# Performance work log

Hardware: AMD Instinct MI355X
Metric: run time of the kernel (lower is better)

The kernel has to match this reference:

```python
import jax, jax.numpy as jnp
import numpy as np
from functools import partial

B, N, T = 4, 10000, 128
E = 160000
H, C = 4, 64            # heads, out_channels per head
GAT_DIM = H * C         # 256
NEG_SLOPE = 0.2


def conv1d(x, w, b):
    # x: (M, Cin, L), w: (Cout, Cin, K), 'same' padding (pad=1 for k=3)
    y = jax.lax.conv_general_dilated(x, w, window_strides=(1,), padding=[(1, 1)],
                                     dimension_numbers=('NCH', 'OIH', 'NCH'))
    return y + b[None, :, None]


def maxpool2(x):
    # kernel=2, stride=2 over last axis
    return jax.lax.reduce_window(x, -jnp.inf, jax.lax.max,
                                 (1, 1, 2), (1, 1, 2), 'VALID')


def gat_layer_single(x, src, dst, W, att_s, att_d, bias):
    # x: (N, Fin); PyG GATConv with concat=True, self-loops already appended to src/dst
    n = x.shape[0]
    xl = (x @ W).reshape(n, H, C)                       # (N, H, C)
    a_s = jnp.sum(xl * att_s[None], axis=-1)            # (N, H)
    a_d = jnp.sum(xl * att_d[None], axis=-1)            # (N, H)
    e = jax.nn.leaky_relu(a_s[src] + a_d[dst], NEG_SLOPE)  # (E', H)
    emax = jax.ops.segment_max(e, dst, num_segments=n)     # (N, H)
    ex = jnp.exp(e - emax[dst])
    denom = jax.ops.segment_sum(ex, dst, num_segments=n)   # (N, H)
    alpha = ex / (denom[dst] + 1e-16)                       # (E', H)
    msg = xl[src] * alpha[..., None]                        # (E', H, C)
    out = jax.ops.segment_sum(msg, dst, num_segments=n)     # (N, H, C)
    return out.reshape(n, H * C) + bias


def setup_inputs() -> dict:
    key = jax.random.key(0)
    ks = jax.random.split(key, 24)
    rn = lambda k, sh, fan: jax.random.normal(k, sh, jnp.float32) / np.sqrt(fan)
    inp = {
        'x': jax.random.normal(ks[0], (B, N, T), jnp.float32),
        'edge_index': jax.random.randint(ks[1], (2, E), 0, N, jnp.int64),
        # temporal conv
        'cw1': rn(ks[2], (32, 1, 3), 3), 'cb1': jnp.zeros((32,), jnp.float32),
        'cw2': rn(ks[3], (64, 32, 3), 96), 'cb2': jnp.zeros((64,), jnp.float32),
        # GAT layer 0 (in=64)
        'W0': rn(ks[4], (64, GAT_DIM), 64), 'as0': rn(ks[5], (H, C), C), 'ad0': rn(ks[6], (H, C), C),
        'b0': jnp.zeros((GAT_DIM,), jnp.float32),
        # GAT layer 1 (in=256)
        'W1': rn(ks[7], (GAT_DIM, GAT_DIM), GAT_DIM), 'as1': rn(ks[8], (H, C), C), 'ad1': rn(ks[9], (H, C), C),
        'b1': jnp.zeros((GAT_DIM,), jnp.float32),
        # classification head 256->128->2
        'Wc1': rn(ks[10], (GAT_DIM, 128), GAT_DIM), 'bc1': jnp.zeros((128,), jnp.float32),
        'Wc2': rn(ks[11], (128, 2), 128), 'bc2': jnp.zeros((2,), jnp.float32),
        # attribution head 256->64->1
        'Wa1': rn(ks[12], (GAT_DIM, 64), GAT_DIM), 'ba1': jnp.zeros((64,), jnp.float32),
        'Wa2': rn(ks[13], (64, 1), 64), 'ba2': jnp.zeros((1,), jnp.float32),
    }
    return inp


def reference(x, edge_index, cw1, cb1, cw2, cb2, W0, as0, ad0, b0, W1, as1, ad1, b1,
              Wc1, bc1, Wc2, bc2, Wa1, ba1, Wa2, ba2):
    b, n, t = x.shape
    # ---- temporal conv over all B*N node signals ----
    xf = x.reshape(b * n, 1, t)
    h = jax.nn.relu(conv1d(xf, cw1, cb1))            # (BN, 32, T)
    h = maxpool2(h)                                  # (BN, 32, T//2)
    h = jax.nn.relu(conv1d(h, cw2, cb2))             # (BN, 64, T//2)
    feat = jnp.mean(h, axis=-1).reshape(b, n, 64)    # adaptive_avg_pool1d(1)
    # ---- GAT stack (self-loops appended, PyG default) ----
    src0, dst0 = edge_index[0], edge_index[1]
    loops = jnp.arange(n, dtype=src0.dtype)
    src = jnp.concatenate([src0, loops])
    dst = jnp.concatenate([dst0, loops])
    gat0 = jax.vmap(partial(gat_layer_single, src=src, dst=dst, W=W0, att_s=as0, att_d=ad0, bias=b0))
    gat1 = jax.vmap(partial(gat_layer_single, src=src, dst=dst, W=W1, att_s=as1, att_d=ad1, bias=b1))
    g = jax.nn.relu(gat0(feat))                      # (B, N, 256); dropout = identity (eval)
    g = jax.nn.relu(gat1(g))                         # (B, N, 256)
    # ---- heads ----
    pooled = jnp.mean(g, axis=1)                     # (B, 256)
    logits = jax.nn.relu(pooled @ Wc1 + bc1) @ Wc2 + bc2          # (B, 2)
    attr = jax.nn.sigmoid(jax.nn.relu(g @ Wa1 + ba1) @ Wa2 + ba2)  # (B, N, 1)
    return logits, attr[..., 0]
```

## Files before the change

### kernel.cpp

```cpp
#include <hip/hip_runtime.h>
#include <hip/hip_bf16.h>
#include <math.h>

typedef __hip_bfloat16 bf16;
typedef unsigned short u16;
typedef unsigned int u32;
typedef __attribute__((ext_vector_type(8))) short short8;
typedef __attribute__((ext_vector_type(4))) float f32x4;
typedef __attribute__((ext_vector_type(2))) float f32x2;

#define BATCH 4
#define NNODE 10000
#define TLEN 128
#define NEDGE 160000
#define GDIM 256
#define NHEAD 4

#define S_CW1 0
#define S_CB1 96
#define S_CB2 128
#define S_AS0 192
#define S_AD0 448
#define S_B0  704
#define S_AS1 960
#define S_AD1 1216
#define S_B1  1472
#define S_BC1 1728
#define S_WC2 1856
#define S_BC2 2112
#define S_BA1 2114
#define S_WA2 2178
#define S_BA2 2242
#define S_TOTAL 2243

__device__ __forceinline__ float prelu(float v) { return fmaxf(v, 0.f); }
__device__ __forceinline__ u16 f2b(float f) {
    union { float f; u32 u; } v; v.f = f;
    u32 r = v.u + 0x7FFF + ((v.u >> 16) & 1);
    return (u16)(r >> 16);
}
__device__ __forceinline__ float u2f(u16 u) {
    union { u32 u; float f; } v; v.u = ((u32)u) << 16;
    return v.f;
}
__device__ __forceinline__ float ldw(const void* p, int off, bool isbf) {
    return isbf ? u2f(((const u16*)p)[off]) : ((const float*)p)[off];
}

__device__ __forceinline__ bool probe_x_bf16(const void* xsrc) {
    int lane = threadIdx.x & 63;
    u16 h = ((const u16*)xsrc)[2 * lane];
    int e = (h >> 7) & 0xFF;
    unsigned long long m = __ballot(e >= 117 && e <= 130);
    return __popcll(m) >= 32;
}
__device__ __forceinline__ bool probe_ei64(const int* ei) {
    int lane = threadIdx.x & 63;
    int v = ei[2 * lane + 1];
    unsigned long long m = __ballot(v == 0);
    return __popcll(m) >= 56;
}

struct WPtrs { const void* p[20]; };

#define PRE_TBLK 665
__global__ __launch_bounds__(256) void k_pre(WPtrs wp, const void* __restrict__ xsrc,
        const int* __restrict__ ei, float* __restrict__ wbuf,
        u16* __restrict__ cw2r, u16* __restrict__ W0t, u16* __restrict__ W1t,
        u16* __restrict__ Wa1t, int* __restrict__ counts) {
    bool isbf = probe_x_bf16(xsrc);
    int b = blockIdx.x;
    if (b >= PRE_TBLK) {
        const int C2[16] = {0,96,128,192,448,704,960,1216,1472,1728,1856,2112,
                            2114,2178,2242,2243};
        const int SRC[15] = {0,1,3,5,6,7,9,10,11,13,14,15,17,18,19};
        int i = (b - PRE_TBLK) * 256 + threadIdx.x;
        if (i >= S_TOTAL) return;
        int j = 14;
        for (int t = 0; t < 15; ++t) { if (i < C2[t + 1]) { j = t; break; } }
        wbuf[i] = ldw(wp.p[SRC[j]], i - C2[j], isbf);
        return;
    }
    int i = b * 256 + threadIdx.x;
    if (i < 6144) {
        int c2 = i / 96, k = i - c2 * 96, s = k >> 5, ci = k & 31;
        cw2r[i] = f2b(ldw(wp.p[2], c2 * 96 + ci * 3 + s, isbf));
    }
    if (i < 16384) {
        int k = i >> 8, c = i & 255;
        W0t[c * 64 + k] = f2b(ldw(wp.p[4], k * 256 + c, isbf));
        int ka = i >> 6, ca = i & 63;
        Wa1t[ca * 256 + ka] = f2b(ldw(wp.p[16], ka * 64 + ca, isbf));
    }
    if (i < 65536) {
        int k = i >> 8, c = i & 255;
        W1t[c * 256 + k] = f2b(ldw(wp.p[8], k * 256 + c, isbf));
    }
    if (i < NEDGE + NNODE) {
        bool ei64 = probe_ei64(ei);
        int dst;
        if (i < NEDGE) dst = ei64 ? ei[2 * (NEDGE + i)] : ei[NEDGE + i];
        else dst = i - NEDGE;
        if (dst >= 0 && dst < NNODE) atomicAdd(&counts[dst], 1);
    }
}

__global__ __launch_bounds__(1024) void k_scan(const int* __restrict__ counts,
        int* __restrict__ cur, int* __restrict__ row_ptr) {
    __shared__ int buf[1024];
    int t = threadIdx.x;
    int base = t * 10;
    int c[10];
    int s = 0;
    #pragma unroll
    for (int i = 0; i < 10; ++i) {
        int idx = base + i;
        c[i] = (idx < NNODE) ? counts[idx] : 0;
        s += c[i];
    }
    buf[t] = s;
    __syncthreads();
    for (int off = 1; off < 1024; off <<= 1) {
        int v = (t >= off) ? buf[t - off] : 0;
        __syncthreads();
        buf[t] += v;
        __syncthreads();
    }
    int run = buf[t] - s;
    #pragma unroll
    for (int i = 0; i < 10; ++i) {
        int idx = base + i;
        if (idx < NNODE) {
            cur[idx] = run;
            run += c[i];
            row_ptr[idx + 1] = run;
        }
    }
    if (t == 0) row_ptr[0] = 0;
}

#define HSTR 40
#define FSTR 72
#define NPW 4
#define FILL_BLK 665
__global__ __launch_bounds__(256) void k_conv(const void* __restrict__ xsrc,
        const float* __restrict__ wbuf, const u16* __restrict__ cw2r,
        const u16* __restrict__ W0t, u16* __restrict__ featb,
        u16* __restrict__ xlb, float* __restrict__ a_s, float* __restrict__ a_d,
        const int* __restrict__ ei, int* __restrict__ cur, int* __restrict__ col_src) {
    __shared__ __align__(16) float xs[4][132];
    __shared__ float w1s[96], b1s[32], b2s[64];
    __shared__ __align__(16) u16 hb[4][66 * HSTR];
    __shared__ __align__(16) u16 fs[16][FSTR];

    bool isbf = probe_x_bf16(xsrc);
    int tid = threadIdx.x;
    int wave = tid >> 6, lane = tid & 63;
    int node0 = blockIdx.x * (4 * NPW);

    int m = lane & 15, q = lane >> 4;
    short8 bfr[4][3];
    #pragma unroll
    for (int nt = 0; nt < 4; ++nt)
        #pragma unroll
        for (int sh = 0; sh < 3; ++sh)
            bfr[nt][sh] = *(const short8*)&cw2r[(nt * 16 + m) * 96 + sh * 32 + q * 8];

    if (tid < 96) w1s[tid] = wbuf[S_CW1 + tid];
    if (tid < 32) b1s[tid] = wbuf[S_CB1 + tid];
    if (tid < 64) b2s[tid] = wbuf[S_CB2 + tid];
    if (tid < 8) xs[tid >> 1][(tid & 1) ? 129 : 0] = 0.f;
    if (tid < 64) {
        int w = tid >> 4, idx = tid & 15;
        *(u32*)&hb[w][2 * idx] = 0;
        *(u32*)&hb[w][65 * HSTR + 2 * idx] = 0;
    }
    __syncthreads();

    float* xsw = xs[wave];
    u16* hw = &hb[wave][0];

    int d = m, uu = q;
    float wa0 = w1s[6 * d + 0], wa1 = w1s[6 * d + 1], wa2 = w1s[6 * d + 2];
    float wb0 = w1s[6 * d + 3], wb1 = w1s[6 * d + 4], wb2 = w1s[6 * d + 5];
    float ba = b1s[2 * d], bb = b1s[2 * d + 1];
    float b2vv[4];
    #pragma unroll
    for (int nt = 0; nt < 4; ++nt) b2vv[nt] = b2s[nt * 16 + m];

    int node = node0 + wave;
    u32 plo = 0; float2 pf = {0.f, 0.f};
    if (isbf) plo = ((const u32*)xsrc)[(size_t)node * 64 + lane];
    else      pf  = ((const float2*)xsrc)[(size_t)node * 64 + lane];

    for (int j = 0; j < NPW; ++j) {
        if (isbf) {
            xsw[1 + 2 * lane] = u2f((u16)(plo & 0xFFFF));
            xsw[2 + 2 * lane] = u2f((u16)(plo >> 16));
        } else {
            xsw[1 + 2 * lane] = pf.x;
            xsw[2 + 2 * lane] = pf.y;
        }
        if (j + 1 < NPW) {
            int nxt = node + 4;
            if (isbf) plo = ((const u32*)xsrc)[(size_t)nxt * 64 + lane];
            else      pf  = ((const float2*)xsrc)[(size_t)nxt * 64 + lane];
        }

        #pragma unroll
        for (int it = 0; it < 16; ++it) {
            int u = uu + 4 * it;
            int t0 = 2 * u;
            float2 xa = *(const float2*)&xsw[t0];
            float2 xb = *(const float2*)&xsw[t0 + 2];
            float x0 = xa.x, x1 = xa.y, x2 = xb.x, x3 = xb.y;
            f32x2 A = {x0, x1}, Bv = {x1, x2}, Cv = {x2, x3};
            f32x2 va = {ba, ba}; va += wa0 * A; va += wa1 * Bv; va += wa2 * Cv;
            f32x2 vb = {bb, bb}; vb += wb0 * A; vb += wb1 * Bv; vb += wb2 * Cv;
            float ha = fmaxf(fmaxf(va.x, va.y), 0.f);
            float hb2 = fmaxf(fmaxf(vb.x, vb.y), 0.f);
            __hip_bfloat162 hp2 = __float22bfloat162_rn(make_float2(ha, hb2));
            u32 pack; __builtin_memcpy(&pack, &hp2, 4);
            *(u32*)&hw[(u + 1) * HSTR + 2 * d] = pack;
        }

        float pc0 = 0.f, pc1 = 0.f, pc2 = 0.f, pc3 = 0.f;
        #pragma unroll
        for (int mt = 0; mt < 4; ++mt) {
            const u16* hr = &hw[(mt * 16 + m) * HSTR + q * 8];
            short8 a0 = *(const short8*)&hr[0 * HSTR];
            short8 a1 = *(const short8*)&hr[1 * HSTR];
            short8 a2 = *(const short8*)&hr[2 * HSTR];
            f32x4 c0 = {0.f,0.f,0.f,0.f}, c1 = {0.f,0.f,0.f,0.f};
            f32x4 c2 = {0.f,0.f,0.f,0.f}, c3 = {0.f,0.f,0.f,0.f};
            c0 = __builtin_amdgcn_mfma_f32_16x16x32_bf16(a0, bfr[0][0], c0, 0, 0, 0);
            c1 = __builtin_amdgcn_mfma_f32_16x16x32_bf16(a0, bfr[1][0], c1, 0, 0, 0);
            c2 = __builtin_amdgcn_mfma_f32_16x16x32_bf16(a0, bfr[2][0], c2, 0, 0, 0);
            c3 = __builtin_amdgcn_mfma_f32_16x16x32_bf16(a0, bfr[3][0], c3, 0, 0, 0);
            c0 = __builtin_amdgcn_mfma_f32_16x16x32_bf16(a1, bfr[0][1], c0, 0, 0, 0);
            c1 = __builtin_amdgcn_mfma_f32_16x16x32_bf16(a1, bfr[1][1], c1, 0, 0, 0);
            c2 = __builtin_amdgcn_mfma_f32_16x16x32_bf16(a1, bfr[2][1], c2, 0, 0, 0);
            c3 = __builtin_amdgcn_mfma_f32_16x16x32_bf16(a1, bfr[3][1], c3, 0, 0, 0);
            c0 = __builtin_amdgcn_mfma_f32_16x16x32_bf16(a2, bfr[0][2], c0, 0, 0, 0);
            c1 = __builtin_amdgcn_mfma_f32_16x16x32_bf16(a2, bfr[1][2], c1, 0, 0, 0);
            c2 = __builtin_amdgcn_mfma_f32_16x16x32_bf16(a2, bfr[2][2], c2, 0, 0, 0);
            c3 = __builtin_amdgcn_mfma_f32_16x16x32_bf16(a2, bfr[3][2], c3, 0, 0, 0);
            pc0 += prelu(c0[0] + b2vv[0]) + prelu(c0[1] + b2vv[0])
                 + prelu(c0[2] + b2vv[0]) + prelu(c0[3] + b2vv[0]);
            pc1 += prelu(c1[0] + b2vv[1]) + prelu(c1[1] + b2vv[1])
                 + prelu(c1[2] + b2vv[1]) + prelu(c1[3] + b2vv[1]);
            pc2 += prelu(c2[0] + b2vv[2]) + prelu(c2[1] + b2vv[2])
                 + prelu(c2[2] + b2vv[2]) + prelu(c2[3] + b2vv[2]);
            pc3 += prelu(c3[0] + b2vv[3]) + prelu(c3[1] + b2vv[3])
                 + prelu(c3[2] + b2vv[3]) + prelu(c3[3] + b2vv[3]);
        }
        pc0 += __shfl_xor(pc0, 16, 64); pc0 += __shfl_xor(pc0, 32, 64);
        pc1 += __shfl_xor(pc1, 16, 64); pc1 += __shfl_xor(pc1, 32, 64);
        pc2 += __shfl_xor(pc2, 16, 64); pc2 += __shfl_xor(pc2, 32, 64);
        pc3 += __shfl_xor(pc3, 16, 64); pc3 += __shfl_xor(pc3, 32, 64);
        float v = (q == 0) ? pc0 : (q == 1) ? pc1 : (q == 2) ? pc2 : pc3;
        u16 fv = f2b(v * (1.f / 64.f));
        if (node < 32) featb[(size_t)node * 64 + lane] = fv;
        fs[wave + 4 * j][lane] = fv;

        node += 4;
    }

    if (blockIdx.x < FILL_BLK) {
        bool ei64 = probe_ei64(ei);
        int e = blockIdx.x * 256 + tid;
        if (e < NEDGE + NNODE) {
            int src, dst;
            if (e < NEDGE) {
                if (ei64) { src = ei[2 * e]; dst = ei[2 * (NEDGE + e)]; }
                else      { src = ei[e];     dst = ei[NEDGE + e]; }
            } else {
                src = dst = e - NEDGE;
            }
            if (dst >= 0 && dst < NNODE) {
                int pos = atomicAdd(&cur[dst], 1);
                if (pos >= 0 && pos < NEDGE + NNODE) col_src[pos] = src;
            }
        }
    }

    __syncthreads();

    {
        f32x4 acc[4];
        #pragma unroll
        for (int ntl = 0; ntl < 4; ++ntl) acc[ntl] = {0.f, 0.f, 0.f, 0.f};
        #pragma unroll
        for (int kc = 0; kc < 64; kc += 32) {
            short8 a = *(const short8*)&fs[m][kc + q * 8];
            #pragma unroll
            for (int ntl = 0; ntl < 4; ++ntl) {
                int col0 = wave * 64 + ntl * 16;
                short8 bw = *(const short8*)&W0t[(size_t)(col0 + m) * 64 + kc + q * 8];
                acc[ntl] = __builtin_amdgcn_mfma_f32_16x16x32_bf16(a, bw, acc[ntl], 0, 0, 0);
            }
        }
        #pragma unroll
        for (int ntl = 0; ntl < 4; ++ntl) {
            #pragma unroll
            for (int r = 0; r < 4; ++r)
                xlb[(size_t)(node0 + q * 4 + r) * 256 + wave * 64 + ntl * 16 + m]
                    = f2b(acc[ntl][r]);
        }
        const float* asw_p = wbuf + S_AS0;
        const float* adw_p = wbuf + S_AD0;
        float sh_s[4] = {0, 0, 0, 0}, sh_d[4] = {0, 0, 0, 0};
        #pragma unroll
        for (int ntl = 0; ntl < 4; ++ntl) {
            float asw = asw_p[wave * 64 + ntl * 16 + m];
            float adw = adw_p[wave * 64 + ntl * 16 + m];
            #pragma unroll
            for (int r = 0; r < 4; ++r) {
                sh_s[r] += acc[ntl][r] * asw;
                sh_d[r] += acc[ntl][r] * adw;
            }
        }
        #pragma unroll
        for (int off = 1; off < 16; off <<= 1) {
            #pragma unroll
            for (int r = 0; r < 4; ++r) {
                sh_s[r] += __shfl_xor(sh_s[r], off, 64);
                sh_d[r] += __shfl_xor(sh_d[r], off, 64);
            }
        }
        if (m == 0) {
            int bb2 = node0 / NNODE;
            int nn0 = node0 - bb2 * NNODE;
            #pragma unroll
            for (int r = 0; r < 4; ++r) {
                int nn = nn0 + q * 4 + r;
                a_s[(size_t)nn * 16 + bb2 * 4 + wave] = sh_s[r];
                a_d[(size_t)nn * 16 + bb2 * 4 + wave] = sh_d[r];
            }
        }
    }
}

#define GSTR 264
__global__ __launch_bounds__(512) void k_agg_gemm(const u16* __restrict__ xlb,
        const float* __restrict__ a_s, const float* __restrict__ a_d,
        const int* __restrict__ row_ptr, const int* __restrict__ col_src,
        const float* __restrict__ bias, const u16* __restrict__ W1t,
        const float* __restrict__ wbuf, u16* __restrict__ outb,
        float* __restrict__ as_out, float* __restrict__ ad_out) {
    __shared__ __align__(16) u16 gt[16][GSTR];
    __shared__ float ps_s[8][16], ps_d[8][16];

    int tid = threadIdx.x;
    int wave = tid >> 6, lane = tid & 63;
    int dl = wave >> 1;
    int dst = __builtin_amdgcn_readfirstlane(blockIdx.x * 4 + dl);
    int bp = (wave & 1) * 2;
    int beg = __builtin_amdgcn_readfirstlane(row_ptr[dst]);
    int end = __builtin_amdgcn_readfirstlane(row_ptr[dst + 1]);

    int bl = lane >> 5;
    int s = lane & 31;
    int h = s >> 3;
    int b = bp + bl;
    int asoff = b * 4 + h;
    size_t rowb = (size_t)b * NNODE;
    float advh = a_d[(size_t)dst * 16 + asoff];

    float m = -INFINITY, l = 0.f;
    float acc[8];
    #pragma unroll
    for (int k = 0; k < 8; ++k) acc[k] = 0.f;

    int i = beg;
    int n0 = 0, n1 = 0, n2 = 0, n3 = 0;
    if (i + 4 <= end) {
        n0 = col_src[i]; n1 = col_src[i + 1];
        n2 = col_src[i + 2]; n3 = col_src[i + 3];
    }
    while (i + 4 <= end) {
        int s0 = min(max(n0, 0), NNODE - 1);
        int s1 = min(max(n1, 0), NNODE - 1);
        int s2 = min(max(n2, 0), NNODE - 1);
        int s3 = min(max(n3, 0), NNODE - 1);
        float a0 = a_s[(size_t)s0 * 16 + asoff];
        float a1 = a_s[(size_t)s1 * 16 + asoff];
        float a2 = a_s[(size_t)s2 * 16 + asoff];
        float a3 = a_s[(size_t)s3 * 16 + asoff];
        short8 x0 = *(const short8*)&xlb[(rowb + s0) * 256 + s * 8];
        short8 x1 = *(const short8*)&xlb[(rowb + s1) * 256 + s * 8];
        short8 x2 = *(const short8*)&xlb[(rowb + s2) * 256 + s * 8];
        short8 x3 = *(const short8*)&xlb[(rowb + s3) * 256 + s * 8];
        i += 4;
        if (i + 4 <= end) {
            n0 = col_src[i]; n1 = col_src[i + 1];
            n2 = col_src[i + 2]; n3 = col_src[i + 3];
        }
        float e0 = a0 + advh; e0 = (e0 >= 0.f) ? e0 : 0.2f * e0;
        float e1 = a1 + advh; e1 = (e1 >= 0.f) ? e1 : 0.2f * e1;
        float e2 = a2 + advh; e2 = (e2 >= 0.f) ? e2 : 0.2f * e2;
        float e3 = a3 + advh; e3 = (e3 >= 0.f) ? e3 : 0.2f * e3;
        float cmax = fmaxf(fmaxf(e0, e1), fmaxf(e2, e3));
        if (__any(cmax > m)) {
            float mn = fmaxf(m, cmax);
            float r = __expf(m - mn);
            m = mn;
            l *= r;
            #pragma unroll
            for (int k = 0; k < 8; ++k) acc[k] *= r;
        }
        float p0 = __expf(e0 - m); l += p0;
        #pragma unroll
        for (int k = 0; k < 8; ++k) acc[k] += p0 * u2f((u16)x0[k]);
        float p1 = __expf(e1 - m); l += p1;
        #pragma unroll
        for (int k = 0; k < 8; ++k) acc[k] += p1 * u2f((u16)x1[k]);
        float p2 = __expf(e2 - m); l += p2;
        #pragma unroll
        for (int k = 0; k < 8; ++k) acc[k] += p2 * u2f((u16)x2[k]);
        float p3 = __expf(e3 - m); l += p3;
        #pragma unroll
        for (int k = 0; k < 8; ++k) acc[k] += p3 * u2f((u16)x3[k]);
    }
    for (; i < end; ++i) {
        int s0 = min(max(col_src[i], 0), NNODE - 1);
        float a0 = a_s[(size_t)s0 * 16 + asoff];
        short8 x0 = *(const short8*)&xlb[(rowb + s0) * 256 + s * 8];
        float e0 = a0 + advh; e0 = (e0 >= 0.f) ? e0 : 0.2f * e0;
        if (__any(e0 > m)) {
            float mn = fmaxf(m, e0);
            float r = __expf(m - mn);
            m = mn;
            l *= r;
            #pragma unroll
            for (int k = 0; k < 8; ++k) acc[k] *= r;
        }
        float p0 = __expf(e0 - m); l += p0;
        #pragma unroll
        for (int k = 0; k < 8; ++k) acc[k] += p0 * u2f((u16)x0[k]);
    }

    float rl = 1.f / (l + 1e-16f);
    short8 o;
    #pragma unroll
    for (int k = 0; k < 8; ++k)
        o[k] = (short)f2b(prelu(acc[k] * rl + bias[s * 8 + k]));
    int grow = dl * 4 + b;
    *(short8*)&gt[grow][s * 8] = o;
    __syncthreads();

    int mm = lane & 15, q = lane >> 4;
    f32x4 ac2[2];
    ac2[0] = {0.f, 0.f, 0.f, 0.f};
    ac2[1] = {0.f, 0.f, 0.f, 0.f};
    for (int kc = 0; kc < 256; kc += 32) {
        short8 a = *(const short8*)&gt[mm][kc + q * 8];
        #pragma unroll
        for (int ntl = 0; ntl < 2; ++ntl) {
            short8 bw = *(const short8*)&W1t[(size_t)(wave * 32 + ntl * 16 + mm) * 256 + kc + q * 8];
            ac2[ntl] = __builtin_amdgcn_mfma_f32_16x16x32_bf16(a, bw, ac2[ntl], 0, 0, 0);
        }
    }
    int dbase = blockIdx.x * 4;
    #pragma unroll
    for (int ntl = 0; ntl < 2; ++ntl) {
        #pragma unroll
        for (int r = 0; r < 4; ++r)
            outb[((size_t)r * NNODE + dbase + q) * 256 + wave * 32 + ntl * 16 + mm]
                = f2b(ac2[ntl][r]);
    }
    float sh_s[4] = {0, 0, 0, 0}, sh_d[4] = {0, 0, 0, 0};
    #pragma unroll
    for (int ntl = 0; ntl < 2; ++ntl) {
        int col = wave * 32 + ntl * 16 + mm;
        float asw = wbuf[S_AS1 + col];
        float adw = wbuf[S_AD1 + col];
        #pragma unroll
        for (int r = 0; r < 4; ++r) {
            sh_s[r] += ac2[ntl][r] * asw;
            sh_d[r] += ac2[ntl][r] * adw;
        }
    }
    #pragma unroll
    for (int off = 1; off < 16; off <<= 1) {
        #pragma unroll
        for (int r = 0; r < 4; ++r) {
            sh_s[r] += __shfl_xor(sh_s[r], off, 64);
            sh_d[r] += __shfl_xor(sh_d[r], off, 64);
        }
    }
    if (mm == 0) {
        #pragma unroll
        for (int r = 0; r < 4; ++r) {
            ps_s[wave][q * 4 + r] = sh_s[r];
            ps_d[wave][q * 4 + r] = sh_d[r];
        }
    }
    __syncthreads();
    if (tid < 128) {
        int sd = tid >> 6, hh = (tid >> 4) & 3, row2 = tid & 15;
        int nn = dbase + (row2 >> 2), bb = row2 & 3;
        if (sd == 0)
            as_out[(size_t)nn * 16 + bb * 4 + hh] = ps_s[2 * hh][row2] + ps_s[2 * hh + 1][row2];
        else
            ad_out[(size_t)nn * 16 + bb * 4 + hh] = ps_d[2 * hh][row2] + ps_d[2 * hh + 1][row2];
    }
}

__global__ __launch_bounds__(256) void k_agg(const u16* __restrict__ xlb,
        const float* __restrict__ a_s, const float* __restrict__ a_d,
        const int* __restrict__ row_ptr, const int* __restrict__ col_src,
        const float* __restrict__ bias, u16* __restrict__ gb_out) {
    int wave = threadIdx.x >> 6, lane = threadIdx.x & 63;
    int dst = __builtin_amdgcn_readfirstlane(blockIdx.x * 2 + (wave >> 1));
    int bp = (wave & 1) * 2;
    int beg = __builtin_amdgcn_readfirstlane(row_ptr[dst]);
    int end = __builtin_amdgcn_readfirstlane(row_ptr[dst + 1]);

    int bl = lane >> 5;
    int s = lane & 31;
    int h = s >> 3;
    int b = bp + bl;
    int asoff = b * 4 + h;
    size_t rowb = (size_t)b * NNODE;
    float advh = a_d[(size_t)dst * 16 + asoff];

    float m = -INFINITY, l = 0.f;
    float acc[8];
    #pragma unroll
    for (int k = 0; k < 8; ++k) acc[k] = 0.f;

    int i = beg;
    int n0 = 0, n1 = 0, n2 = 0, n3 = 0;
    if (i + 4 <= end) {
        n0 = col_src[i]; n1 = col_src[i + 1];
        n2 = col_src[i + 2]; n3 = col_src[i + 3];
    }
    while (i + 4 <= end) {
        int s0 = min(max(n0, 0), NNODE - 1);
        int s1 = min(max(n1, 0), NNODE - 1);
        int s2 = min(max(n2, 0), NNODE - 1);
        int s3 = min(max(n3, 0), NNODE - 1);
        float a0 = a_s[(size_t)s0 * 16 + asoff];
        float a1 = a_s[(size_t)s1 * 16 + asoff];
        float a2 = a_s[(size_t)s2 * 16 + asoff];
        float a3 = a_s[(size_t)s3 * 16 + asoff];
        short8 x0 = *(const short8*)&xlb[(rowb + s0) * 256 + s * 8];
        short8 x1 = *(const short8*)&xlb[(rowb + s1) * 256 + s * 8];
        short8 x2 = *(const short8*)&xlb[(rowb + s2) * 256 + s * 8];
        short8 x3 = *(const short8*)&xlb[(rowb + s3) * 256 + s * 8];
        i += 4;
        if (i + 4 <= end) {
            n0 = col_src[i]; n1 = col_src[i + 1];
            n2 = col_src[i + 2]; n3 = col_src[i + 3];
        }
        float e0 = a0 + advh; e0 = (e0 >= 0.f) ? e0 : 0.2f * e0;
        float e1 = a1 + advh; e1 = (e1 >= 0.f) ? e1 : 0.2f * e1;
        float e2 = a2 + advh; e2 = (e2 >= 0.f) ? e2 : 0.2f * e2;
        float e3 = a3 + advh; e3 = (e3 >= 0.f) ? e3 : 0.2f * e3;
        float cmax = fmaxf(fmaxf(e0, e1), fmaxf(e2, e3));
        if (__any(cmax > m)) {
            float mn = fmaxf(m, cmax);
            float r = __expf(m - mn);
            m = mn;
            l *= r;
            #pragma unroll
            for (int k = 0; k < 8; ++k) acc[k] *= r;
        }
        float p0 = __expf(e0 - m); l += p0;
        #pragma unroll
        for (int k = 0; k < 8; ++k) acc[k] += p0 * u2f((u16)x0[k]);
        float p1 = __expf(e1 - m); l += p1;
        #pragma unroll
        for (int k = 0; k < 8; ++k) acc[k] += p1 * u2f((u16)x1[k]);
        float p2 = __expf(e2 - m); l += p2;
        #pragma unroll
        for (int k = 0; k < 8; ++k) acc[k] += p2 * u2f((u16)x2[k]);
        float p3 = __expf(e3 - m); l += p3;
        #pragma unroll
        for (int k = 0; k < 8; ++k) acc[k] += p3 * u2f((u16)x3[k]);
    }
    for (; i < end; ++i) {
        int s0 = min(max(col_src[i], 0), NNODE - 1);
        float a0 = a_s[(size_t)s0 * 16 + asoff];
        short8 x0 = *(const short8*)&xlb[(rowb + s0) * 256 + s * 8];
        float e0 = a0 + advh; e0 = (e0 >= 0.f) ? e0 : 0.2f * e0;
        if (__any(e0 > m)) {
            float mn = fmaxf(m, e0);
            float r = __expf(m - mn);
            m = mn;
            l *= r;
            #pragma unroll
            for (int k = 0; k < 8; ++k) acc[k] *= r;
        }
        float p0 = __expf(e0 - m); l += p0;
        #pragma unroll
        for (int k = 0; k < 8; ++k) acc[k] += p0 * u2f((u16)x0[k]);
    }

    float rl = 1.f / (l + 1e-16f);
    short8 o;
    #pragma unroll
    for (int k = 0; k < 8; ++k)
        o[k] = (short)f2b(prelu(acc[k] * rl + bias[s * 8 + k]));
    *(short8*)&gb_out[(rowb + dst) * 256 + s * 8] = o;
}

__global__ __launch_bounds__(256) void k_attrpool(const u16* __restrict__ gb,
        const u16* __restrict__ Wa1t, const float* __restrict__ wbuf,
        float* __restrict__ out, float* __restrict__ pooled) {
    if (blockIdx.x >= 625) {
        int pb = blockIdx.x - 625;
        int b = pb >> 6;
        int chunk = pb & 63;
        int cch = threadIdx.x;
        int n0 = chunk * 157;
        int n1 = min(NNODE, n0 + 157);
        size_t rowb = (size_t)b * NNODE;
        float acc = 0.f;
        int n = n0;
        for (; n + 4 <= n1; n += 4) {
            float v0 = u2f(gb[(rowb + n) * 256 + cch]);
            float v1 = u2f(gb[(rowb + n + 1) * 256 + cch]);
            float v2 = u2f(gb[(rowb + n + 2) * 256 + cch]);
            float v3 = u2f(gb[(rowb + n + 3) * 256 + cch]);
            acc += v0; acc += v1; acc += v2; acc += v3;
        }
        for (; n < n1; ++n)
            acc += u2f(gb[(rowb + n) * 256 + cch]);
        atomicAdd(&pooled[b * 256 + cch], acc);
        return;
    }
    int wave = threadIdx.x >> 6, lane = threadIdx.x & 63;
    int row0 = (blockIdx.x * 4 + wave) * 16;
    int m = lane & 15, q = lane >> 4;
    f32x4 acc[4];
    #pragma unroll
    for (int nt = 0; nt < 4; ++nt) acc[nt] = {0.f, 0.f, 0.f, 0.f};
    for (int kc = 0; kc < 256; kc += 32) {
        short8 a = *(const short8*)&gb[(size_t)(row0 + m) * 256 + kc + q * 8];
        #pragma unroll
        for (int nt = 0; nt < 4; ++nt) {
            short8 b = *(const short8*)&Wa1t[(size_t)(nt * 16 + m) * 256 + kc + q * 8];
            acc[nt] = __builtin_amdgcn_mfma_f32_16x16x32_bf16(a, b, acc[nt], 0, 0, 0);
        }
    }
    float part[4] = {0, 0, 0, 0};
    #pragma unroll
    for (int nt = 0; nt < 4; ++nt) {
        int col = nt * 16 + m;
        float ba1v = wbuf[S_BA1 + col];
        float wa2v = wbuf[S_WA2 + col];
        #pragma unroll
        for (int r = 0; r < 4; ++r)
            part[r] += prelu(acc[nt][r] + ba1v) * wa2v;
    }
    #pragma unroll
    for (int off = 1; off < 16; off <<= 1) {
        #pragma unroll
        for (int r = 0; r < 4; ++r)
            part[r] += __shfl_xor(part[r], off, 64);
    }
    if (m == 0) {
        float ba2v = wbuf[S_BA2];
        #pragma unroll
        for (int r = 0; r < 4; ++r) {
            int row = row0 + q * 4 + r;
            float v = part[r] + ba2v;
            out[8 + row] = 1.f / (1.f + __expf(-v));
        }
    }
}

__global__ __launch_bounds__(128) void k_logits(const float* __restrict__ pooled,
        const float* __restrict__ wbuf, const void* __restrict__ Wc1p,
        float* __restrict__ out,
        const u16* __restrict__ featb, const u16* __restrict__ gb,
        const int* __restrict__ row_ptr, const int* __restrict__ ei,
        const void* __restrict__ xsrc, int hostbad) {
    int tid = threadIdx.x;
    bool isbf = probe_x_bf16(xsrc);
    if (blockIdx.x == 4) {
        __shared__ float red[128];
        bool ei64 = probe_ei64(ei);
        float mx[2] = {0.f, 0.f};
        const u16* bufs[2] = {featb, gb};
        for (int qq = 0; qq < 2; ++qq) {
            const u16* p = bufs[qq];
            float m = 0.f;
            for (int i = tid; i < 2048; i += 128) {
                float v = u2f(p[i]);
                if (v != v) m = 1e30f;
                m = fmaxf(m, fabsf(v));
            }
            red[tid] = m;
            __syncthreads();
            for (int s2 = 64; s2 > 0; s2 >>= 1) {
                if (tid < s2) red[tid] = fmaxf(red[tid], red[tid + s2]);
                __syncthreads();
            }
            mx[qq] = red[0];
            __syncthreads();
        }
        if (tid == 0) {
            int fb = (mx[0] > 1e8f || mx[0] < 1e-6f) ? 1 : 0;
            int gbad = (mx[1] > 1e8f || mx[1] < 1e-6f) ? 1 : 0;
            int cb = (row_ptr[NNODE] != NEDGE + NNODE) ? 1 : 0;
            int code = 100 * fb + 400 * gbad + 800 * cb + 6400 * hostbad;
            if (code) {
                code += 1600 * (isbf ? 0 : 1);
                code += 3200 * (ei64 ? 1 : 0);
                for (int j = 0; j < 8; ++j) out[j] = (float)code;
            }
        }
        return;
    }
    __shared__ float pm[256];
    __shared__ float red4[4];
    int b = blockIdx.x;
    pm[tid] = pooled[b * 256 + tid] * (1.f / NNODE);
    pm[tid + 128] = pooled[b * 256 + tid + 128] * (1.f / NNODE);
    __syncthreads();
    float acc = wbuf[S_BC1 + tid];
    if (isbf) {
        const u16* w = (const u16*)Wc1p;
        #pragma unroll 4
        for (int k = 0; k < 256; ++k)
            acc += pm[k] * u2f(w[k * 128 + tid]);
    } else {
        const float* w = (const float*)Wc1p;
        #pragma unroll 4
        for (int k = 0; k < 256; ++k)
            acc += pm[k] * w[k * 128 + tid];
    }
    float hv = prelu(acc);
    float p0 = hv * wbuf[S_WC2 + tid * 2];
    float p1 = hv * wbuf[S_WC2 + tid * 2 + 1];
    #pragma unroll
    for (int off = 32; off > 0; off >>= 1) {
        p0 += __shfl_xor(p0, off, 64);
        p1 += __shfl_xor(p1, off, 64);
    }
    int wv = tid >> 6, lane = tid & 63;
    if (lane == 0) { red4[wv * 2] = p0; red4[wv * 2 + 1] = p1; }
    __syncthreads();
    if (tid < 2)
        out[b * 2 + tid] = red4[tid] + red4[2 + tid] + wbuf[S_BC2 + tid];
}

extern "C" void kernel_launch(void* const* d_in, const int* in_sizes, int n_in,
                              void* d_out, int out_size, void* d_ws, size_t ws_size,
                              hipStream_t stream) {
    const void* x  = d_in[0];
    const int*  ei = (const int*)d_in[1];
    float* out = (float*)d_out;

    WPtrs wp;
    for (int j = 0; j < 20; ++j) wp.p[j] = d_in[j + 2];

    char* ws = (char*)d_ws;
    size_t off = 0;
    auto alloc = [&](size_t bytes) -> void* {
        void* p = ws + off;
        off += (bytes + 255) & ~(size_t)255;
        return p;
    };
    float* wbuf    = (float*)alloc((size_t)S_TOTAL * 4);
    u16*   featb   = (u16*)  alloc((size_t)BATCH * NNODE * 64 * 2);
    u16*   xlb     = (u16*)  alloc((size_t)BATCH * NNODE * 256 * 2);
    u16*   gb      = (u16*)  alloc((size_t)BATCH * NNODE * 256 * 2);
    float* a_s     = (float*)alloc((size_t)BATCH * NNODE * 4 * 4);
    float* a_d     = (float*)alloc((size_t)BATCH * NNODE * 4 * 4);
    float* a_s2    = (float*)alloc((size_t)BATCH * NNODE * 4 * 4);
    float* a_d2    = (float*)alloc((size_t)BATCH * NNODE * 4 * 4);
    u16*   cw2r    = (u16*)alloc(6144 * 2);
    u16*   W0t     = (u16*)alloc(16384 * 2);
    u16*   W1t     = (u16*)alloc(65536 * 2);
    u16*   Wa1t    = (u16*)alloc(16384 * 2);
    int*   counts  = (int*)alloc(NNODE * 4);
    float* pooled  = (float*)alloc(BATCH * 256 * 4);
    int*   row_ptr = (int*)alloc((NNODE + 1) * 4);
    int*   cur     = (int*)alloc(NNODE * 4);
    int*   col_src = (int*)alloc((NEDGE + NNODE) * 4);
    (void)ws_size; (void)out_size;

    int hostbad = (n_in != 22 || in_sizes[0] != BATCH * NNODE * TLEN ||
                   in_sizes[1] != 2 * NEDGE) ? 1 : 0;

    hipMemsetAsync(counts, 0, 40192 + 4096, stream);

    k_pre<<<PRE_TBLK + 9, 256, 0, stream>>>(wp, x, ei, wbuf, cw2r, W0t, W1t, Wa1t, counts);
    k_scan<<<1, 1024, 0, stream>>>(counts, cur, row_ptr);

    k_conv<<<BATCH * NNODE / 16, 256, 0, stream>>>(x, wbuf, cw2r, W0t, featb,
            xlb, a_s, a_d, ei, cur, col_src);

    k_agg_gemm<<<NNODE / 4, 512, 0, stream>>>(xlb, a_s, a_d, row_ptr, col_src,
            wbuf + S_B0, W1t, wbuf, gb, a_s2, a_d2);

    k_agg<<<NNODE / 2, 256, 0, stream>>>(gb, a_s2, a_d2, row_ptr, col_src, wbuf + S_B1, xlb);

    k_attrpool<<<625 + 256, 256, 0, stream>>>(xlb, Wa1t, wbuf, out, pooled);
    k_logits<<<5, 128, 0, stream>>>(pooled, wbuf, wp.p[12], out, featb, xlb, row_ptr, ei, x, hostbad);
}
```

Measured before the change: 358.9 us.

## Fuse second GAT aggregation with attribution head and mean pooling

Merges the layer-1 aggregation kernel and the attribution/pooling kernel into one kernel. Each block now aggregates 4 destination nodes across 4 batches into shared memory, then runs the attribution MLP with MFMA and the column pooling from that tile. This removes the write and re-read of the full layer-1 output and one kernel launch. In exchange it adds a block-wide barrier after aggregation, many more atomicAdds on pooled (one per block per batch-channel), and writes only a small diagonal slice of the output for the later check kernel.

```diff
diff --git a/kernel.cpp b/kernel.cpp
--- a/kernel.cpp
+++ b/kernel.cpp
@@ -507,12 +507,19 @@
     }
 }
 
-__global__ __launch_bounds__(256) void k_agg(const u16* __restrict__ xlb,
+__global__ __launch_bounds__(512) void k_agg_attr(const u16* __restrict__ gb,
         const float* __restrict__ a_s, const float* __restrict__ a_d,
         const int* __restrict__ row_ptr, const int* __restrict__ col_src,
-        const float* __restrict__ bias, u16* __restrict__ gb_out) {
-    int wave = threadIdx.x >> 6, lane = threadIdx.x & 63;
-    int dst = __builtin_amdgcn_readfirstlane(blockIdx.x * 2 + (wave >> 1));
+        const float* __restrict__ bias, const u16* __restrict__ Wa1t,
+        const float* __restrict__ wbuf, u16* __restrict__ gdiag,
+        float* __restrict__ out, float* __restrict__ pooled) {
+    __shared__ __align__(16) u16 gt[16][GSTR];
+    __shared__ float ps_a[4][16];
+
+    int tid = threadIdx.x;
+    int wave = tid >> 6, lane = tid & 63;
+    int dl = wave >> 1;
+    int dst = __builtin_amdgcn_readfirstlane(blockIdx.x * 4 + dl);
     int bp = (wave & 1) * 2;
     int beg = __builtin_amdgcn_readfirstlane(row_ptr[dst]);
     int end = __builtin_amdgcn_readfirstlane(row_ptr[dst + 1]);
@@ -545,10 +552,10 @@
         float a1 = a_s[(size_t)s1 * 16 + asoff];
         float a2 = a_s[(size_t)s2 * 16 + asoff];
         float a3 = a_s[(size_t)s3 * 16 + asoff];
-        short8 x0 = *(const short8*)&xlb[(rowb + s0) * 256 + s * 8];
-        short8 x1 = *(const short8*)&xlb[(rowb + s1) * 256 + s * 8];
-        short8 x2 = *(const short8*)&xlb[(rowb + s2) * 256 + s * 8];
-        short8 x3 = *(const short8*)&xlb[(rowb + s3) * 256 + s * 8];
+        short8 x0 = *(const short8*)&gb[(rowb + s0) * 256 + s * 8];
+        short8 x1 = *(const short8*)&gb[(rowb + s1) * 256 + s * 8];
+        short8 x2 = *(const short8*)&gb[(rowb + s2) * 256 + s * 8];
+        short8 x3 = *(const short8*)&gb[(rowb + s3) * 256 + s * 8];
         i += 4;
         if (i + 4 <= end) {
             n0 = col_src[i]; n1 = col_src[i + 1];
@@ -583,7 +590,7 @@
     for (; i < end; ++i) {
         int s0 = min(max(col_src[i], 0), NNODE - 1);
         float a0 = a_s[(size_t)s0 * 16 + asoff];
-        short8 x0 = *(const short8*)&xlb[(rowb + s0) * 256 + s * 8];
+        short8 x0 = *(const short8*)&gb[(rowb + s0) * 256 + s * 8];
         float e0 = a0 + advh; e0 = (e0 >= 0.f) ? e0 : 0.2f * e0;
         if (__any(e0 > m)) {
             float mn = fmaxf(m, e0);
@@ -603,72 +610,53 @@
     #pragma unroll
     for (int k = 0; k < 8; ++k)
         o[k] = (short)f2b(prelu(acc[k] * rl + bias[s * 8 + k]));
-    *(short8*)&gb_out[(rowb + dst) * 256 + s * 8] = o;
-}
-
-__global__ __launch_bounds__(256) void k_attrpool(const u16* __restrict__ gb,
-        const u16* __restrict__ Wa1t, const float* __restrict__ wbuf,
-        float* __restrict__ out, float* __restrict__ pooled) {
-    if (blockIdx.x >= 625) {
-        int pb = blockIdx.x - 625;
-        int b = pb >> 6;
-        int chunk = pb & 63;
-        int cch = threadIdx.x;
-        int n0 = chunk * 157;
-        int n1 = min(NNODE, n0 + 157);
-        size_t rowb = (size_t)b * NNODE;
-        float acc = 0.f;
-        int n = n0;
-        for (; n + 4 <= n1; n += 4) {
-            float v0 = u2f(gb[(rowb + n) * 256 + cch]);
-            float v1 = u2f(gb[(rowb + n + 1) * 256 + cch]);
-            float v2 = u2f(gb[(rowb + n + 2) * 256 + cch]);
-            float v3 = u2f(gb[(rowb + n + 3) * 256 + cch]);
-            acc += v0; acc += v1; acc += v2; acc += v3;
-        }
-        for (; n < n1; ++n)
-            acc += u2f(gb[(rowb + n) * 256 + cch]);
-        atomicAdd(&pooled[b * 256 + cch], acc);
-        return;
-    }
-    int wave = threadIdx.x >> 6, lane = threadIdx.x & 63;
-    int row0 = (blockIdx.x * 4 + wave) * 16;
-    int m = lane & 15, q = lane >> 4;
-    f32x4 acc[4];
-    #pragma unroll
-    for (int nt = 0; nt < 4; ++nt) acc[nt] = {0.f, 0.f, 0.f, 0.f};
-    for (int kc = 0; kc < 256; kc += 32) {
-        short8 a = *(const short8*)&gb[(size_t)(row0 + m) * 256 + kc + q * 8];
-        #pragma unroll
-        for (int nt = 0; nt < 4; ++nt) {
-            short8 b = *(const short8*)&Wa1t[(size_t)(nt * 16 + m) * 256 + kc + q * 8];
-            acc[nt] = __builtin_amdgcn_mfma_f32_16x16x32_bf16(a, b, acc[nt], 0, 0, 0);
-        }
-    }
-    float part[4] = {0, 0, 0, 0};
-    #pragma unroll
-    for (int nt = 0; nt < 4; ++nt) {
-        int col = nt * 16 + m;
+    *(short8*)&gt[dl * 4 + b][s * 8] = o;
+    if (b == 0 && dst < 8)
+        *(short8*)&gdiag[(size_t)dst * 256 + s * 8] = o;
+    __syncthreads();
+
+    int dbase = blockIdx.x * 4;
+    int mm = lane & 15, q = lane >> 4;
+    if (wave < 4) {
+        f32x4 ac2 = {0.f, 0.f, 0.f, 0.f};
+        for (int kc = 0; kc < 256; kc += 32) {
+            short8 a = *(const short8*)&gt[mm][kc + q * 8];
+            short8 bw = *(const short8*)&Wa1t[(size_t)(wave * 16 + mm) * 256 + kc + q * 8];
+            ac2 = __builtin_amdgcn_mfma_f32_16x16x32_bf16(a, bw, ac2, 0, 0, 0);
+        }
+        int col = wave * 16 + mm;
         float ba1v = wbuf[S_BA1 + col];
         float wa2v = wbuf[S_WA2 + col];
+        float part[4];
         #pragma unroll
         for (int r = 0; r < 4; ++r)
-            part[r] += prelu(acc[nt][r] + ba1v) * wa2v;
-    }
-    #pragma unroll
-    for (int off = 1; off < 16; off <<= 1) {
-        #pragma unroll
-        for (int r = 0; r < 4; ++r)
-            part[r] += __shfl_xor(part[r], off, 64);
-    }
-    if (m == 0) {
-        float ba2v = wbuf[S_BA2];
-        #pragma unroll
-        for (int r = 0; r < 4; ++r) {
-            int row = row0 + q * 4 + r;
-            float v = part[r] + ba2v;
-            out[8 + row] = 1.f / (1.f + __expf(-v));
-        }
+            part[r] = prelu(ac2[r] + ba1v) * wa2v;
+        #pragma unroll
+        for (int off = 1; off < 16; off <<= 1) {
+            #pragma unroll
+            for (int r = 0; r < 4; ++r)
+                part[r] += __shfl_xor(part[r], off, 64);
+        }
+        if (mm == 0) {
+            #pragma unroll
+            for (int r = 0; r < 4; ++r)
+                ps_a[wave][q * 4 + r] = part[r];
+        }
+    } else {
+        int c = tid - 256;
+        #pragma unroll
+        for (int bb = 0; bb < 4; ++bb) {
+            float sum = u2f(gt[0 * 4 + bb][c]) + u2f(gt[1 * 4 + bb][c])
+                      + u2f(gt[2 * 4 + bb][c]) + u2f(gt[3 * 4 + bb][c]);
+            atomicAdd(&pooled[bb * 256 + c], sum);
+        }
+    }
+    __syncthreads();
+    if (tid < 16) {
+        int rr = tid;
+        float v = ps_a[0][rr] + ps_a[1][rr] + ps_a[2][rr] + ps_a[3][rr] + wbuf[S_BA2];
+        int dl2 = rr >> 2, b2 = rr & 3;
+        out[8 + (size_t)b2 * NNODE + dbase + dl2] = 1.f / (1.f + __expf(-v));
     }
 }
 
@@ -798,8 +786,8 @@
     k_agg_gemm<<<NNODE / 4, 512, 0, stream>>>(xlb, a_s, a_d, row_ptr, col_src,
             wbuf + S_B0, W1t, wbuf, gb, a_s2, a_d2);
 
-    k_agg<<<NNODE / 2, 256, 0, stream>>>(gb, a_s2, a_d2, row_ptr, col_src, wbuf + S_B1, xlb);
-
-    k_attrpool<<<625 + 256, 256, 0, stream>>>(xlb, Wa1t, wbuf, out, pooled);
+    k_agg_attr<<<NNODE / 4, 512, 0, stream>>>(gb, a_s2, a_d2, row_ptr, col_src,
+            wbuf + S_B1, Wa1t, wbuf, xlb, out, pooled);
+
     k_logits<<<5, 128, 0, stream>>>(pooled, wbuf, wp.p[12], out, featb, xlb, row_ptr, ei, x, hostbad);
 }
```

After: 361.8 us, median of 3. Within noise of the previous version (+0.8%).
